# Kernel optimization log

Hardware: AMD Instinct MI355X
Metric: run time of the kernel (lower is better)

Reference implementation:

```python
import jax, jax.numpy as jnp
import numpy as np

B, L, D, H, HS, V, NL = 8, 513, 512, 8, 64, 513, 6  # head_size = D // H
EPS = 1e-5


def setup_inputs() -> dict:
    key = jax.random.key(0)
    ks = jax.random.split(key, 8)
    s = 0.02
    return {
        "x": jax.random.randint(ks[0], (B, L), 0, V),
        "embed": jax.random.normal(ks[1], (V, D), jnp.float32) * s,
        "pos_embed": jax.random.normal(ks[2], (L, D), jnp.float32) * s,
        "Wq": jax.random.normal(ks[3], (NL, H, D, HS), jnp.float32) * s,
        "Wk": jax.random.normal(ks[4], (NL, H, D, HS), jnp.float32) * s,
        "Wv": jax.random.normal(ks[5], (NL, H, D, HS), jnp.float32) * s,
        "ln1_g": jnp.ones((NL, D), jnp.float32),
        "ln1_b": jnp.zeros((NL, D), jnp.float32),
        "ln2_g": jnp.ones((NL, D), jnp.float32),
        "ln2_b": jnp.zeros((NL, D), jnp.float32),
        "mlp_W": jax.random.normal(ks[6], (NL, D, D), jnp.float32) * s,
        "mlp_b": jnp.zeros((NL, D), jnp.float32),
        "fc_W": jax.random.normal(ks[7], (D, V), jnp.float32) * s,
        "fc_b": jnp.zeros((V,), jnp.float32),
    }


def _layernorm(x, g, b):
    mu = jnp.mean(x, axis=-1, keepdims=True)
    var = jnp.mean(jnp.square(x - mu), axis=-1, keepdims=True)
    return (x - mu) * jax.lax.rsqrt(var + EPS) * g + b


def reference(x, embed, pos_embed, Wq, Wk, Wv, ln1_g, ln1_b, ln2_g, ln2_b,
              mlp_W, mlp_b, fc_W, fc_b):
    h = embed[x] + pos_embed[None]                       # (B, L, D)
    mask = jnp.tril(jnp.ones((L, L), bool))              # causal tril buffer
    scale = HS ** -0.5
    for i in range(NL):
        xn = _layernorm(h, ln1_g[i], ln1_b[i])
        # all heads batched (original loops per head; same math)
        q = jnp.einsum('bld,hde->bhle', xn, Wq[i])
        k = jnp.einsum('bld,hde->bhle', xn, Wk[i])
        v = jnp.einsum('bld,hde->bhle', xn, Wv[i])
        w = jnp.einsum('bhle,bhme->bhlm', q, k) * scale
        w = jnp.where(mask, w, -jnp.inf)
        w = jax.nn.softmax(w, axis=-1)
        y = jnp.einsum('bhlm,bhme->bhle', w, v)
        y = y.transpose(0, 2, 1, 3).reshape(B, L, D)     # concat heads
        h = y + h
        xn2 = _layernorm(h, ln2_g[i], ln2_b[i])
        h = jax.nn.gelu(xn2 @ mlp_W[i] + mlp_b[i], approximate=False) + h
    return h @ fc_W + fc_b                               # (B, L, V) logits
```

## Files before the change

kernel.cpp:

```cpp
#include <hip/hip_runtime.h>
#include <hip/hip_bf16.h>
#include <math.h>

#define B 8
#define L 513
#define D 512
#define H 8
#define HS 64
#define V 513
#define NL 6
#define BL (B * L)
#define LP 576
#define EPS 1e-5f

typedef __attribute__((ext_vector_type(8))) short bf16x8;
typedef __attribute__((ext_vector_type(4))) float f32x4;

__device__ inline ushort f2b(float f) {
    __hip_bfloat16 h = __float2bfloat16(f);
    return *reinterpret_cast<ushort*>(&h);
}

__global__ __launch_bounds__(256) void embed_k(const int* __restrict__ x,
                                               const float* __restrict__ emb,
                                               const float* __restrict__ pos,
                                               float* __restrict__ hbuf)
{
    int row = blockIdx.x;
    int l   = row % L;
    int tok = x[row];
    const float* er = emb + (size_t)tok * D;
    const float* pr = pos + (size_t)l * D;
    float* hr = hbuf + (size_t)row * D;
    for (int d = threadIdx.x; d < D; d += 256)
        hr[d] = er[d] + pr[d];
}

__global__ __launch_bounds__(64) void ln_k(const float* __restrict__ x,
                                           const float* __restrict__ g,
                                           const float* __restrict__ b,
                                           ushort* __restrict__ o)
{
    const int row = blockIdx.x, lane = threadIdx.x;
    const float* xr = x + (size_t)row * D + lane * 8;
    float4 v0 = *(const float4*)xr;
    float4 v1 = *(const float4*)(xr + 4);
    float s = v0.x + v0.y + v0.z + v0.w + v1.x + v1.y + v1.z + v1.w;
#pragma unroll
    for (int off = 1; off < 64; off <<= 1) s += __shfl_xor(s, off);
    const float mu = s * (1.f / D);
    float d0 = v0.x - mu, d1 = v0.y - mu, d2 = v0.z - mu, d3 = v0.w - mu;
    float d4 = v1.x - mu, d5 = v1.y - mu, d6 = v1.z - mu, d7 = v1.w - mu;
    float ss = d0*d0 + d1*d1 + d2*d2 + d3*d3 + d4*d4 + d5*d5 + d6*d6 + d7*d7;
#pragma unroll
    for (int off = 1; off < 64; off <<= 1) ss += __shfl_xor(ss, off);
    const float rs = rsqrtf(ss * (1.f / D) + EPS);
    const float* gp = g + lane * 8;
    const float* bp = b + lane * 8;
    float4 g0 = *(const float4*)gp, g1 = *(const float4*)(gp + 4);
    float4 b0 = *(const float4*)bp, b1 = *(const float4*)(bp + 4);
    ushort4 u0, u1;
    u0.x = f2b(d0 * rs * g0.x + b0.x); u0.y = f2b(d1 * rs * g0.y + b0.y);
    u0.z = f2b(d2 * rs * g0.z + b0.z); u0.w = f2b(d3 * rs * g0.w + b0.w);
    u1.x = f2b(d4 * rs * g1.x + b1.x); u1.y = f2b(d5 * rs * g1.y + b1.y);
    u1.z = f2b(d6 * rs * g1.z + b1.z); u1.w = f2b(d7 * rs * g1.w + b1.w);
    ushort* orow = o + (size_t)row * D + lane * 8;
    *(ushort4*)orow       = u0;
    *(ushort4*)(orow + 4) = u1;
}

__global__ __launch_bounds__(256) void cvt_qkv_k(const float* __restrict__ Wq,
                                                 const float* __restrict__ Wk,
                                                 const float* __restrict__ Wv,
                                                 ushort* __restrict__ Wp)
{
    const int dc = blockIdx.x;
    const int i  = blockIdx.y / H, h = blockIdx.y % H;
    const int sel = blockIdx.z;
    const float* W = (sel == 0) ? Wq : (sel == 1) ? Wk : Wv;
    const float* src = W + ((size_t)i * H + h) * D * HS + (size_t)dc * 64 * HS;
    __shared__ float T[64][65];
    const int tid = threadIdx.x;
#pragma unroll
    for (int it = 0; it < 4; ++it) {
        int idx = tid + it * 256;
        int r = idx >> 4, e4 = (idx & 15) * 4;
        float4 f = *(const float4*)(src + (size_t)r * HS + e4);
        T[r][e4] = f.x; T[r][e4 + 1] = f.y; T[r][e4 + 2] = f.z; T[r][e4 + 3] = f.w;
    }
    __syncthreads();
    ushort* dst = Wp + (size_t)i * 1536 * 512 + (size_t)(sel * 512 + h * 64) * 512 + dc * 64;
#pragma unroll
    for (int it = 0; it < 4; ++it) {
        int idx = tid + it * 256;
        int e = idx >> 4, d4 = (idx & 15) * 4;
        ushort4 u;
        u.x = f2b(T[d4][e]); u.y = f2b(T[d4 + 1][e]);
        u.z = f2b(T[d4 + 2][e]); u.w = f2b(T[d4 + 3][e]);
        *(ushort4*)(dst + (size_t)e * 512 + d4) = u;
    }
}

__global__ __launch_bounds__(256) void cvt_mlp_k(const float* __restrict__ Wm,
                                                 ushort* __restrict__ Wt)
{
    const int nt = blockIdx.x, kt = blockIdx.y, i = blockIdx.z;
    const float* src = Wm + (size_t)i * D * D;
    __shared__ float T[64][65];
    const int tid = threadIdx.x;
#pragma unroll
    for (int it = 0; it < 4; ++it) {
        int idx = tid + it * 256;
        int r = idx >> 4, e4 = (idx & 15) * 4;
        float4 f = *(const float4*)(src + (size_t)(kt * 64 + r) * D + nt * 64 + e4);
        T[r][e4] = f.x; T[r][e4 + 1] = f.y; T[r][e4 + 2] = f.z; T[r][e4 + 3] = f.w;
    }
    __syncthreads();
    ushort* dst = Wt + (size_t)i * D * D + (size_t)(nt * 64) * D + kt * 64;
#pragma unroll
    for (int it = 0; it < 4; ++it) {
        int idx = tid + it * 256;
        int e = idx >> 4, k4 = (idx & 15) * 4;
        ushort4 u;
        u.x = f2b(T[k4][e]); u.y = f2b(T[k4 + 1][e]);
        u.z = f2b(T[k4 + 2][e]); u.w = f2b(T[k4 + 3][e]);
        *(ushort4*)(dst + (size_t)e * D + k4) = u;
    }
}

__global__ __launch_bounds__(256) void cvt_fc_k(const float* __restrict__ Wf,
                                                ushort* __restrict__ Wt)
{
    const int nt = blockIdx.x, kt = blockIdx.y;
    __shared__ float T[64][65];
    const int tid = threadIdx.x;
#pragma unroll
    for (int it = 0; it < 4; ++it) {
        int idx = tid + it * 256;
        int r = idx >> 4, e4 = (idx & 15) * 4;
#pragma unroll
        for (int j = 0; j < 4; ++j) {
            int n = nt * 64 + e4 + j;
            T[r][e4 + j] = (n < V) ? Wf[(size_t)(kt * 64 + r) * V + n] : 0.f;
        }
    }
    __syncthreads();
    ushort* dst = Wt + (size_t)(nt * 64) * 512 + kt * 64;
#pragma unroll
    for (int it = 0; it < 4; ++it) {
        int idx = tid + it * 256;
        int e = idx >> 4, k4 = (idx & 15) * 4;
        ushort4 u;
        u.x = f2b(T[k4][e]); u.y = f2b(T[k4 + 1][e]);
        u.z = f2b(T[k4 + 2][e]); u.w = f2b(T[k4 + 3][e]);
        *(ushort4*)(dst + (size_t)e * 512 + k4) = u;
    }
}

template <int MODE>
__global__ __launch_bounds__(256) void mgemm_k(const ushort* __restrict__ A,
                                               const ushort* __restrict__ Bt,
                                               const float* __restrict__ bias,
                                               void* __restrict__ o0,
                                               void* __restrict__ o1,
                                               void* __restrict__ o2)
{
    __shared__ ushort As[64][72];
    __shared__ ushort Bs[64][72];
    const int tid  = threadIdx.x;
    const int wave = tid >> 6, lane = tid & 63;
    const int row0 = blockIdx.y * 64;
    const int col0 = blockIdx.x * 64;
    const int wr = (wave >> 1) * 32, wc = (wave & 1) * 32;
    const int frow = lane & 15;
    const int kb   = lane >> 4;

    f32x4 acc[2][2] = {};

    for (int k0 = 0; k0 < 512; k0 += 64) {
#pragma unroll
        for (int it = 0; it < 2; ++it) {
            int idx = tid + it * 256;
            int r = idx >> 3, kc = idx & 7;
            uint4 av = make_uint4(0u, 0u, 0u, 0u);
            if (row0 + r < BL)
                av = *(const uint4*)(A + (size_t)(row0 + r) * 512 + k0 + kc * 8);
            *(uint4*)&As[r][kc * 8] = av;
            uint4 bv = *(const uint4*)(Bt + (size_t)(col0 + r) * 512 + k0 + kc * 8);
            *(uint4*)&Bs[r][kc * 8] = bv;
        }
        __syncthreads();
#pragma unroll
        for (int ks = 0; ks < 2; ++ks) {
            bf16x8 a[2], b[2];
#pragma unroll
            for (int f = 0; f < 2; ++f) {
                a[f] = *(const bf16x8*)&As[wr + f * 16 + frow][ks * 32 + kb * 8];
                b[f] = *(const bf16x8*)&Bs[wc + f * 16 + frow][ks * 32 + kb * 8];
            }
#pragma unroll
            for (int fi = 0; fi < 2; ++fi)
#pragma unroll
                for (int fj = 0; fj < 2; ++fj)
                    acc[fi][fj] = __builtin_amdgcn_mfma_f32_16x16x32_bf16(
                        a[fi], b[fj], acc[fi][fj], 0, 0, 0);
        }
        __syncthreads();
    }

    const int rbase = row0 + wr + (lane >> 4) * 4;
    const int cbase = col0 + wc + (lane & 15);
#pragma unroll
    for (int fi = 0; fi < 2; ++fi) {
#pragma unroll
        for (int fj = 0; fj < 2; ++fj) {
            const int c = cbase + fj * 16;
#pragma unroll
            for (int rg = 0; rg < 4; ++rg) {
                const int r = rbase + fi * 16 + rg;
                if (r >= BL) continue;
                float val = acc[fi][fj][rg];
                if (MODE == 0) {
                    int buf = c >> 9, cc = c & 511;
                    int b_ = r / L, l = r % L;
                    int head = cc >> 6, e = cc & 63;
                    int bh = b_ * H + head;
                    if (buf == 0)
                        ((ushort*)o0)[((size_t)bh * L + l) * HS + e] = f2b(val);
                    else if (buf == 1)
                        ((ushort*)o1)[((size_t)bh * L + l) * HS + e] = f2b(val);
                    else
                        ((ushort*)o2)[((size_t)bh * HS + e) * LP + l] = f2b(val);
                } else if (MODE == 1) {
                    float xv = val + bias[c];
                    float gl = 0.5f * xv * (1.f + erff(xv * 0.70710678118654752f));
                    ((float*)o0)[(size_t)r * D + c] = gl + ((float*)o0)[(size_t)r * D + c];
                } else if (MODE == 3) {
                    float xv = val + bias[c];
                    float gl = 0.5f * xv * (1.f + erff(xv * 0.70710678118654752f));
                    float res = ((const float*)o1)[(size_t)r * D + c];
                    ((ushort*)o0)[(size_t)r * D + c] = f2b(gl + res);
                } else {
                    if (c < V) ((float*)o0)[(size_t)r * V + c] = val + bias[c];
                }
            }
        }
    }
}

__global__ __launch_bounds__(256) void fattn_k(const ushort* __restrict__ qb,
                                               const ushort* __restrict__ kb,
                                               const ushort* __restrict__ vT,
                                               float* __restrict__ hbuf)
{
    __shared__ ushort Qs[64][72];
    __shared__ ushort Ks[64][72];
    __shared__ ushort Vs[64][72];
    __shared__ ushort Ps[64][72];

    const int bx  = blockIdx.x;
    const int bh  = bx / 9;
    const int qt  = 8 - (bx % 9);
    const int q0  = qt * 64;
    const int tid = threadIdx.x;
    const int wave = tid >> 6, lane = tid & 63;
    const int lg = lane >> 4, li = lane & 15;
    const int wq = wave * 16;

#pragma unroll
    for (int it = 0; it < 2; ++it) {
        int idx = tid + it * 256;
        int r = idx >> 3, c8 = (idx & 7) * 8;
        int qr = q0 + r;
        uint4 val = make_uint4(0u, 0u, 0u, 0u);
        if (qr < L) val = *(const uint4*)(qb + ((size_t)bh * L + qr) * HS + c8);
        *(uint4*)&Qs[r][c8] = val;
    }

    const short one_b = (short)0x3F80;
    const bf16x8 ones = { one_b, one_b, one_b, one_b, one_b, one_b, one_b, one_b };

    f32x4 accO[4] = {};
    f32x4 accL = {};

    const int n_mt = qt + 1;
    uint4 kr[2], vr[2];

    auto loadKV = [&](int t) {
#pragma unroll
        for (int it = 0; it < 2; ++it) {
            int idx = tid + it * 256;
            int r = idx >> 3, c8 = (idx & 7) * 8;
            int mr = t * 64 + r;
            kr[it] = make_uint4(0u, 0u, 0u, 0u);
            if (mr < L) kr[it] = *(const uint4*)(kb + ((size_t)bh * L + mr) * HS + c8);
            vr[it] = *(const uint4*)(vT + ((size_t)bh * HS + r) * LP + t * 64 + c8);
        }
    };
    auto writeKV = [&]() {
#pragma unroll
        for (int it = 0; it < 2; ++it) {
            int idx = tid + it * 256;
            int r = idx >> 3, c8 = (idx & 7) * 8;
            *(uint4*)&Ks[r][c8] = kr[it];
            *(uint4*)&Vs[r][c8] = vr[it];
        }
    };

    loadKV(0);
    writeKV();
    __syncthreads();

    for (int t = 0; t < n_mt; ++t) {
        if (t + 1 < n_mt) loadKV(t + 1);

        f32x4 accS[4] = {};
#pragma unroll
        for (int ks = 0; ks < 2; ++ks) {
            bf16x8 a = *(const bf16x8*)&Qs[wq + li][ks * 32 + lg * 8];
#pragma unroll
            for (int j = 0; j < 4; ++j) {
                bf16x8 b = *(const bf16x8*)&Ks[j * 16 + li][ks * 32 + lg * 8];
                accS[j] = __builtin_amdgcn_mfma_f32_16x16x32_bf16(a, b, accS[j], 0, 0, 0);
            }
        }

        const int m0 = t * 64;
#pragma unroll
        for (int rg = 0; rg < 4; ++rg) {
            const int qrow = q0 + wq + lg * 4 + rg;
#pragma unroll
            for (int j = 0; j < 4; ++j) {
                int mcol = m0 + j * 16 + li;
                float p = (mcol > qrow || mcol >= L) ? 0.f : __expf(accS[j][rg] * 0.125f);
                Ps[wq + lg * 4 + rg][j * 16 + li] = f2b(p);
            }
        }

#pragma unroll
        for (int ks = 0; ks < 2; ++ks) {
            bf16x8 a = *(const bf16x8*)&Ps[wq + li][ks * 32 + lg * 8];
            accL = __builtin_amdgcn_mfma_f32_16x16x32_bf16(a, ones, accL, 0, 0, 0);
#pragma unroll
            for (int j = 0; j < 4; ++j) {
                bf16x8 b = *(const bf16x8*)&Vs[j * 16 + li][ks * 32 + lg * 8];
                accO[j] = __builtin_amdgcn_mfma_f32_16x16x32_bf16(a, b, accO[j], 0, 0, 0);
            }
        }
        __syncthreads();
        if (t + 1 < n_mt) {
            writeKV();
            __syncthreads();
        }
    }

    const int b_ = bh / H, hh = bh % H;
#pragma unroll
    for (int rg = 0; rg < 4; ++rg) {
        const int qrow = q0 + wq + lg * 4 + rg;
        if (qrow >= L) continue;
        const float inv = 1.f / accL[rg];
        float* dst = hbuf + ((size_t)b_ * L + qrow) * D + hh * HS;
#pragma unroll
        for (int j = 0; j < 4; ++j)
            dst[j * 16 + li] += accO[j][rg] * inv;
    }
}

extern "C" void kernel_launch(void* const* d_in, const int* in_sizes, int n_in,
                              void* d_out, int out_size, void* d_ws, size_t ws_size,
                              hipStream_t stream)
{
    const int*   x    = (const int*)d_in[0];
    const float* emb  = (const float*)d_in[1];
    const float* pos  = (const float*)d_in[2];
    const float* Wq   = (const float*)d_in[3];
    const float* Wk   = (const float*)d_in[4];
    const float* Wv   = (const float*)d_in[5];
    const float* ln1g = (const float*)d_in[6];
    const float* ln1b = (const float*)d_in[7];
    const float* ln2g = (const float*)d_in[8];
    const float* ln2b = (const float*)d_in[9];
    const float* mlpW = (const float*)d_in[10];
    const float* mlpb = (const float*)d_in[11];
    const float* fcW  = (const float*)d_in[12];
    const float* fcb  = (const float*)d_in[13];
    float* out = (float*)d_out;

    char* ws = (char*)d_ws;
    float*  h   = (float*)ws;    ws += (size_t)BL * D * 4;
    ushort* qb  = (ushort*)ws;   ws += (size_t)BL * D * 2;
    ushort* kbuf= (ushort*)ws;   ws += (size_t)BL * D * 2;
    ushort* vT  = (ushort*)ws;   ws += (size_t)B * H * HS * LP * 2;
    ushort* xnb = (ushort*)ws;   ws += (size_t)BL * D * 2;
    ushort* hb  = (ushort*)ws;   ws += (size_t)BL * D * 2;
    ushort* Wp  = (ushort*)ws;   ws += (size_t)NL * 1536 * 512 * 2;
    ushort* Wtm = (ushort*)ws;   ws += (size_t)NL * D * D * 2;
    ushort* Wtf = (ushort*)ws;   ws += (size_t)576 * 512 * 2;

    cvt_qkv_k<<<dim3(8, NL * H, 3), 256, 0, stream>>>(Wq, Wk, Wv, Wp);
    cvt_mlp_k<<<dim3(8, 8, NL), 256, 0, stream>>>(mlpW, Wtm);
    cvt_fc_k<<<dim3(9, 8), 256, 0, stream>>>(fcW, Wtf);

    embed_k<<<BL, 256, 0, stream>>>(x, emb, pos, h);

    for (int i = 0; i < NL; ++i) {
        ln_k<<<BL, 64, 0, stream>>>(h, ln1g + i * D, ln1b + i * D, xnb);
        mgemm_k<0><<<dim3(24, 65), 256, 0, stream>>>(
            xnb, Wp + (size_t)i * 1536 * 512, nullptr, qb, kbuf, vT);
        fattn_k<<<B * H * 9, 256, 0, stream>>>(qb, kbuf, vT, h);
        ln_k<<<BL, 64, 0, stream>>>(h, ln2g + i * D, ln2b + i * D, xnb);
        if (i < NL - 1)
            mgemm_k<1><<<dim3(8, 65), 256, 0, stream>>>(
                xnb, Wtm + (size_t)i * D * D, mlpb + i * D, h, nullptr, nullptr);
        else
            mgemm_k<3><<<dim3(8, 65), 256, 0, stream>>>(
                xnb, Wtm + (size_t)i * D * D, mlpb + i * D, hb, h, nullptr);
    }
    mgemm_k<2><<<dim3(9, 65), 256, 0, stream>>>(hb, Wtf, fcb, out, nullptr, nullptr);
}
```

Measured before the change: 574.6 us.

## Double-buffer LDS tiles with XOR swizzle, fuse embed into layernorm, pack LN rows

After: 665.7 us. +15.9%, slower.

```diff
diff --git a/kernel.cpp b/kernel.cpp
--- a/kernel.cpp
+++ b/kernel.cpp
@@ -21,30 +21,9 @@
     return *reinterpret_cast<ushort*>(&h);
 }
 
-__global__ __launch_bounds__(256) void embed_k(const int* __restrict__ x,
-                                               const float* __restrict__ emb,
-                                               const float* __restrict__ pos,
-                                               float* __restrict__ hbuf)
-{
-    int row = blockIdx.x;
-    int l   = row % L;
-    int tok = x[row];
-    const float* er = emb + (size_t)tok * D;
-    const float* pr = pos + (size_t)l * D;
-    float* hr = hbuf + (size_t)row * D;
-    for (int d = threadIdx.x; d < D; d += 256)
-        hr[d] = er[d] + pr[d];
-}
-
-__global__ __launch_bounds__(64) void ln_k(const float* __restrict__ x,
-                                           const float* __restrict__ g,
-                                           const float* __restrict__ b,
-                                           ushort* __restrict__ o)
-{
-    const int row = blockIdx.x, lane = threadIdx.x;
-    const float* xr = x + (size_t)row * D + lane * 8;
-    float4 v0 = *(const float4*)xr;
-    float4 v1 = *(const float4*)(xr + 4);
+__device__ inline void ln_row(float4 v0, float4 v1, const float* g,
+                              const float* b, int lane, ushort* orow)
+{
     float s = v0.x + v0.y + v0.z + v0.w + v1.x + v1.y + v1.z + v1.w;
 #pragma unroll
     for (int off = 1; off < 64; off <<= 1) s += __shfl_xor(s, off);
@@ -64,9 +43,45 @@
     u0.z = f2b(d2 * rs * g0.z + b0.z); u0.w = f2b(d3 * rs * g0.w + b0.w);
     u1.x = f2b(d4 * rs * g1.x + b1.x); u1.y = f2b(d5 * rs * g1.y + b1.y);
     u1.z = f2b(d6 * rs * g1.z + b1.z); u1.w = f2b(d7 * rs * g1.w + b1.w);
-    ushort* orow = o + (size_t)row * D + lane * 8;
     *(ushort4*)orow       = u0;
     *(ushort4*)(orow + 4) = u1;
+}
+
+__global__ __launch_bounds__(256) void ln4_k(const float* __restrict__ x,
+                                             const float* __restrict__ g,
+                                             const float* __restrict__ b,
+                                             ushort* __restrict__ o)
+{
+    const int wave = threadIdx.x >> 6, lane = threadIdx.x & 63;
+    const int row = blockIdx.x * 4 + wave;
+    const float* xr = x + (size_t)row * D + lane * 8;
+    float4 v0 = *(const float4*)xr;
+    float4 v1 = *(const float4*)(xr + 4);
+    ln_row(v0, v1, g, b, lane, o + (size_t)row * D + lane * 8);
+}
+
+__global__ __launch_bounds__(256) void ln_embed4_k(const int* __restrict__ xi,
+                                                   const float* __restrict__ emb,
+                                                   const float* __restrict__ pos,
+                                                   const float* __restrict__ g,
+                                                   const float* __restrict__ b,
+                                                   float* __restrict__ h,
+                                                   ushort* __restrict__ o)
+{
+    const int wave = threadIdx.x >> 6, lane = threadIdx.x & 63;
+    const int row = blockIdx.x * 4 + wave;
+    const int l = row % L;
+    const int tok = xi[row];
+    const float* er = emb + (size_t)tok * D + lane * 8;
+    const float* pr = pos + (size_t)l * D + lane * 8;
+    float4 e0 = *(const float4*)er, e1 = *(const float4*)(er + 4);
+    float4 p0 = *(const float4*)pr, p1 = *(const float4*)(pr + 4);
+    float4 v0 = make_float4(e0.x + p0.x, e0.y + p0.y, e0.z + p0.z, e0.w + p0.w);
+    float4 v1 = make_float4(e1.x + p1.x, e1.y + p1.y, e1.z + p1.z, e1.w + p1.w);
+    float* hr = h + (size_t)row * D + lane * 8;
+    *(float4*)hr       = v0;
+    *(float4*)(hr + 4) = v1;
+    ln_row(v0, v1, g, b, lane, o + (size_t)row * D + lane * 8);
 }
 
 __global__ __launch_bounds__(256) void cvt_qkv_k(const float* __restrict__ Wq,
@@ -165,8 +180,8 @@
                                                void* __restrict__ o1,
                                                void* __restrict__ o2)
 {
-    __shared__ ushort As[64][72];
-    __shared__ ushort Bs[64][72];
+    __shared__ ushort As[2][64 * 64];
+    __shared__ ushort Bs[2][64 * 64];
     const int tid  = threadIdx.x;
     const int wave = tid >> 6, lane = tid & 63;
     const int row0 = blockIdx.y * 64;
@@ -175,28 +190,48 @@
     const int frow = lane & 15;
     const int kb   = lane >> 4;
 
+    uint4 rga[2], rgb[2];
+    const int sr0 = tid >> 3, skc = tid & 7;
+    const int sr1 = (tid + 256) >> 3;
+
+    auto loadAB = [&](int k0) {
+        rga[0] = make_uint4(0u, 0u, 0u, 0u);
+        if (row0 + sr0 < BL)
+            rga[0] = *(const uint4*)(A + (size_t)(row0 + sr0) * 512 + k0 + skc * 8);
+        rgb[0] = *(const uint4*)(Bt + (size_t)(col0 + sr0) * 512 + k0 + skc * 8);
+        rga[1] = make_uint4(0u, 0u, 0u, 0u);
+        if (row0 + sr1 < BL)
+            rga[1] = *(const uint4*)(A + (size_t)(row0 + sr1) * 512 + k0 + skc * 8);
+        rgb[1] = *(const uint4*)(Bt + (size_t)(col0 + sr1) * 512 + k0 + skc * 8);
+    };
+    auto writeAB = [&](int buf) {
+        const int s0 = (skc ^ (sr0 & 7)) * 8;
+        *(uint4*)&As[buf][sr0 * 64 + s0] = rga[0];
+        *(uint4*)&Bs[buf][sr0 * 64 + s0] = rgb[0];
+        const int s1 = (skc ^ (sr1 & 7)) * 8;
+        *(uint4*)&As[buf][sr1 * 64 + s1] = rga[1];
+        *(uint4*)&Bs[buf][sr1 * 64 + s1] = rgb[1];
+    };
+
     f32x4 acc[2][2] = {};
 
-    for (int k0 = 0; k0 < 512; k0 += 64) {
-#pragma unroll
-        for (int it = 0; it < 2; ++it) {
-            int idx = tid + it * 256;
-            int r = idx >> 3, kc = idx & 7;
-            uint4 av = make_uint4(0u, 0u, 0u, 0u);
-            if (row0 + r < BL)
-                av = *(const uint4*)(A + (size_t)(row0 + r) * 512 + k0 + kc * 8);
-            *(uint4*)&As[r][kc * 8] = av;
-            uint4 bv = *(const uint4*)(Bt + (size_t)(col0 + r) * 512 + k0 + kc * 8);
-            *(uint4*)&Bs[r][kc * 8] = bv;
-        }
-        __syncthreads();
+    loadAB(0);
+    writeAB(0);
+    __syncthreads();
+
+    for (int kt = 0; kt < 8; ++kt) {
+        if (kt < 7) loadAB((kt + 1) * 64);
+        const int cur = kt & 1;
 #pragma unroll
         for (int ks = 0; ks < 2; ++ks) {
             bf16x8 a[2], b[2];
+            const int g = ks * 4 + kb;
 #pragma unroll
             for (int f = 0; f < 2; ++f) {
-                a[f] = *(const bf16x8*)&As[wr + f * 16 + frow][ks * 32 + kb * 8];
-                b[f] = *(const bf16x8*)&Bs[wc + f * 16 + frow][ks * 32 + kb * 8];
+                const int ra_ = wr + f * 16 + frow;
+                a[f] = *(const bf16x8*)&As[cur][ra_ * 64 + ((g ^ (ra_ & 7)) * 8)];
+                const int rb_ = wc + f * 16 + frow;
+                b[f] = *(const bf16x8*)&Bs[cur][rb_ * 64 + ((g ^ (rb_ & 7)) * 8)];
             }
 #pragma unroll
             for (int fi = 0; fi < 2; ++fi)
@@ -205,7 +240,10 @@
                     acc[fi][fj] = __builtin_amdgcn_mfma_f32_16x16x32_bf16(
                         a[fi], b[fj], acc[fi][fj], 0, 0, 0);
         }
-        __syncthreads();
+        if (kt < 7) {
+            writeAB(cur ^ 1);
+            __syncthreads();
+        }
     }
 
     const int rbase = row0 + wr + (lane >> 4) * 4;
@@ -253,9 +291,9 @@
                                                const ushort* __restrict__ vT,
                                                float* __restrict__ hbuf)
 {
-    __shared__ ushort Qs[64][72];
-    __shared__ ushort Ks[64][72];
-    __shared__ ushort Vs[64][72];
+    __shared__ ushort Qs[64 * 64];
+    __shared__ ushort Ks[2][64 * 64];
+    __shared__ ushort Vs[2][64 * 64];
     __shared__ ushort Ps[64][72];
 
     const int bx  = blockIdx.x;
@@ -267,14 +305,20 @@
     const int lg = lane >> 4, li = lane & 15;
     const int wq = wave * 16;
 
-#pragma unroll
-    for (int it = 0; it < 2; ++it) {
-        int idx = tid + it * 256;
-        int r = idx >> 3, c8 = (idx & 7) * 8;
-        int qr = q0 + r;
-        uint4 val = make_uint4(0u, 0u, 0u, 0u);
-        if (qr < L) val = *(const uint4*)(qb + ((size_t)bh * L + qr) * HS + c8);
-        *(uint4*)&Qs[r][c8] = val;
+    const int sr0 = tid >> 3, skc = tid & 7;
+    const int sr1 = (tid + 256) >> 3;
+    const int ss0 = (skc ^ (sr0 & 7)) * 8;
+    const int ss1 = (skc ^ (sr1 & 7)) * 8;
+
+    {
+        int qr = q0 + sr0;
+        uint4 v = make_uint4(0u, 0u, 0u, 0u);
+        if (qr < L) v = *(const uint4*)(qb + ((size_t)bh * L + qr) * HS + skc * 8);
+        *(uint4*)&Qs[sr0 * 64 + ss0] = v;
+        qr = q0 + sr1;
+        v = make_uint4(0u, 0u, 0u, 0u);
+        if (qr < L) v = *(const uint4*)(qb + ((size_t)bh * L + qr) * HS + skc * 8);
+        *(uint4*)&Qs[sr1 * 64 + ss1] = v;
     }
 
     const short one_b = (short)0x3F80;
@@ -287,40 +331,40 @@
     uint4 kr[2], vr[2];
 
     auto loadKV = [&](int t) {
-#pragma unroll
-        for (int it = 0; it < 2; ++it) {
-            int idx = tid + it * 256;
-            int r = idx >> 3, c8 = (idx & 7) * 8;
-            int mr = t * 64 + r;
-            kr[it] = make_uint4(0u, 0u, 0u, 0u);
-            if (mr < L) kr[it] = *(const uint4*)(kb + ((size_t)bh * L + mr) * HS + c8);
-            vr[it] = *(const uint4*)(vT + ((size_t)bh * HS + r) * LP + t * 64 + c8);
-        }
+        int mr = t * 64 + sr0;
+        kr[0] = make_uint4(0u, 0u, 0u, 0u);
+        if (mr < L) kr[0] = *(const uint4*)(kb + ((size_t)bh * L + mr) * HS + skc * 8);
+        vr[0] = *(const uint4*)(vT + ((size_t)bh * HS + sr0) * LP + t * 64 + skc * 8);
+        mr = t * 64 + sr1;
+        kr[1] = make_uint4(0u, 0u, 0u, 0u);
+        if (mr < L) kr[1] = *(const uint4*)(kb + ((size_t)bh * L + mr) * HS + skc * 8);
+        vr[1] = *(const uint4*)(vT + ((size_t)bh * HS + sr1) * LP + t * 64 + skc * 8);
     };
-    auto writeKV = [&]() {
-#pragma unroll
-        for (int it = 0; it < 2; ++it) {
-            int idx = tid + it * 256;
-            int r = idx >> 3, c8 = (idx & 7) * 8;
-            *(uint4*)&Ks[r][c8] = kr[it];
-            *(uint4*)&Vs[r][c8] = vr[it];
-        }
+    auto writeKV = [&](int buf) {
+        *(uint4*)&Ks[buf][sr0 * 64 + ss0] = kr[0];
+        *(uint4*)&Vs[buf][sr0 * 64 + ss0] = vr[0];
+        *(uint4*)&Ks[buf][sr1 * 64 + ss1] = kr[1];
+        *(uint4*)&Vs[buf][sr1 * 64 + ss1] = vr[1];
     };
 
     loadKV(0);
-    writeKV();
+    writeKV(0);
     __syncthreads();
 
     for (int t = 0; t < n_mt; ++t) {
         if (t + 1 < n_mt) loadKV(t + 1);
+        const int cur = t & 1;
 
         f32x4 accS[4] = {};
 #pragma unroll
         for (int ks = 0; ks < 2; ++ks) {
-            bf16x8 a = *(const bf16x8*)&Qs[wq + li][ks * 32 + lg * 8];
+            const int g = ks * 4 + lg;
+            const int ra_ = wq + li;
+            bf16x8 a = *(const bf16x8*)&Qs[ra_ * 64 + ((g ^ (ra_ & 7)) * 8)];
 #pragma unroll
             for (int j = 0; j < 4; ++j) {
-                bf16x8 b = *(const bf16x8*)&Ks[j * 16 + li][ks * 32 + lg * 8];
+                const int rb_ = j * 16 + li;
+                bf16x8 b = *(const bf16x8*)&Ks[cur][rb_ * 64 + ((g ^ (rb_ & 7)) * 8)];
                 accS[j] = __builtin_amdgcn_mfma_f32_16x16x32_bf16(a, b, accS[j], 0, 0, 0);
             }
         }
@@ -343,13 +387,14 @@
             accL = __builtin_amdgcn_mfma_f32_16x16x32_bf16(a, ones, accL, 0, 0, 0);
 #pragma unroll
             for (int j = 0; j < 4; ++j) {
-                bf16x8 b = *(const bf16x8*)&Vs[j * 16 + li][ks * 32 + lg * 8];
+                const int g = ks * 4 + lg;
+                const int rb_ = j * 16 + li;
+                bf16x8 b = *(const bf16x8*)&Vs[cur][rb_ * 64 + ((g ^ (rb_ & 7)) * 8)];
                 accO[j] = __builtin_amdgcn_mfma_f32_16x16x32_bf16(a, b, accO[j], 0, 0, 0);
             }
         }
-        __syncthreads();
         if (t + 1 < n_mt) {
-            writeKV();
+            writeKV(cur ^ 1);
             __syncthreads();
         }
     }
@@ -402,14 +447,15 @@
     cvt_mlp_k<<<dim3(8, 8, NL), 256, 0, stream>>>(mlpW, Wtm);
     cvt_fc_k<<<dim3(9, 8), 256, 0, stream>>>(fcW, Wtf);
 
-    embed_k<<<BL, 256, 0, stream>>>(x, emb, pos, h);
-
     for (int i = 0; i < NL; ++i) {
-        ln_k<<<BL, 64, 0, stream>>>(h, ln1g + i * D, ln1b + i * D, xnb);
+        if (i == 0)
+            ln_embed4_k<<<BL / 4, 256, 0, stream>>>(x, emb, pos, ln1g, ln1b, h, xnb);
+        else
+            ln4_k<<<BL / 4, 256, 0, stream>>>(h, ln1g + i * D, ln1b + i * D, xnb);
         mgemm_k<0><<<dim3(24, 65), 256, 0, stream>>>(
             xnb, Wp + (size_t)i * 1536 * 512, nullptr, qb, kbuf, vT);
         fattn_k<<<B * H * 9, 256, 0, stream>>>(qb, kbuf, vT, h);
-        ln_k<<<BL, 64, 0, stream>>>(h, ln2g + i * D, ln2b + i * D, xnb);
+        ln4_k<<<BL / 4, 256, 0, stream>>>(h, ln2g + i * D, ln2b + i * D, xnb);
         if (i < NL - 1)
             mgemm_k<1><<<dim3(8, 65), 256, 0, stream>>>(
                 xnb, Wtm + (size_t)i * D * D, mlpb + i * D, h, nullptr, nullptr);
```
